# Kernel tuning notes

Measured on AMD Instinct MI355X. Metric: run time of the kernel, lower is better.

The kernel has to match this reference:

```python
import jax, jax.numpy as jnp
import numpy as np

N = 100000      # nodes
E = 1600000     # edges
D_IN = 256
D_HID = 256
D_OUT = 256
DROP_P = 0.5


def setup_inputs() -> dict:
    key = jax.random.key(0)
    ks = jax.random.split(key, 10)
    s = 1.0 / np.sqrt(D_HID)
    return {
        "z": jax.random.normal(ks[0], (N, D_OUT), jnp.float32),
        "omega": jax.random.normal(ks[1], (N, D_IN), jnp.float32),
        "edge_index": jax.random.randint(ks[2], (2, E), 0, N, jnp.int32),
        "W_lin": jax.random.normal(ks[3], (D_IN, D_HID), jnp.float32) * s,
        "b_lin": jnp.zeros((D_HID,), jnp.float32),
        "W_g1": jax.random.normal(ks[4], (D_HID, D_HID), jnp.float32) * s,
        "b_g1": jnp.zeros((D_HID,), jnp.float32),
        "W_g2": jax.random.normal(ks[5], (D_HID, D_OUT), jnp.float32) * s,
        "b_g2": jnp.zeros((D_OUT,), jnp.float32),
        "mask1": jax.random.bernoulli(ks[6], 1.0 - DROP_P, (N, D_HID)),
        "mask2": jax.random.bernoulli(ks[7], 1.0 - DROP_P, (N, D_HID)),
    }


def _gcn_norm(edge_index):
    # add self-loops, symmetric normalization deg^-1/2 * deg^-1/2
    loop = jnp.arange(N, dtype=edge_index.dtype)
    src = jnp.concatenate([edge_index[0], loop])
    dst = jnp.concatenate([edge_index[1], loop])
    deg = jax.ops.segment_sum(jnp.ones_like(dst, jnp.float32), dst, num_segments=N)
    dinv = jax.lax.rsqrt(deg)  # deg >= 1 because of self-loops
    norm = dinv[src] * dinv[dst]  # [E+N]
    return src, dst, norm


def _gcn_conv(x, W, b, src, dst, norm):
    h = x @ W                                  # [N, d_out]
    msg = h[src] * norm[:, None]               # gather over edges
    out = jax.ops.segment_sum(msg, dst, num_segments=N)  # scatter-add
    return out + b


def _dropout(x, mask):
    return jnp.where(mask, x * (1.0 / (1.0 - DROP_P)), 0.0)


def reference(z, omega, edge_index, W_lin, b_lin, W_g1, b_g1, W_g2, b_g2, mask1, mask2):
    src, dst, norm = _gcn_norm(edge_index)
    # layer 0: Linear + relu + dropout
    h = _dropout(jax.nn.relu(omega @ W_lin + b_lin), mask1)
    # layer 1: GCNConv + relu + dropout
    h = _dropout(jax.nn.relu(_gcn_conv(h, W_g1, b_g1, src, dst, norm)), mask2)
    # layer 2: GCNConv
    h = _gcn_conv(h, W_g2, b_g2, src, dst, norm)
    return z * h
```

## Files before the change

kernel.cpp:

```cpp
#include <hip/hip_runtime.h>
#include <stdint.h>

#define NN 100000
#define EE 1600000
#define DD 256

typedef __bf16 bf16;
typedef __attribute__((ext_vector_type(8))) __bf16 bf16x8;
typedef __attribute__((ext_vector_type(4))) float f32x4;
typedef __attribute__((ext_vector_type(4))) unsigned int u32x4;
typedef __attribute__((ext_vector_type(8))) unsigned short u16x8;

typedef __attribute__((address_space(1))) const unsigned int g_u32c;
typedef __attribute__((address_space(3))) unsigned int lds_u32;

__device__ __forceinline__ float bflo(unsigned int u) {
    union { unsigned int u; float f; } x; x.u = u << 16; return x.f;
}
__device__ __forceinline__ float bfhi(unsigned int u) {
    union { unsigned int u; float f; } x; x.u = u & 0xFFFF0000u; return x.f;
}
__device__ __forceinline__ unsigned short f2bf(float f) {
    return __builtin_bit_cast(unsigned short, (__bf16)f);
}

#define NSUB 128
__global__ __launch_bounds__(256) void count_deg_k(
    const int* __restrict__ dst, int* __restrict__ cnt) {
    int bid = blockIdx.x;
    int prt = bid & 7;
    int sub = bid >> 3;
    int lo = prt * (NN >> 3);
    int hi = (prt == 7) ? NN : lo + (NN >> 3);
    const int per = EE / NSUB;
    int e0 = sub * per;
    int e1 = (sub == NSUB - 1) ? EE : e0 + per;
    for (int e = e0 + threadIdx.x; e < e1; e += 256) {
        int d = dst[e];
        if (d >= lo && d < hi) atomicAdd(&cnt[d], 1);
    }
}
__global__ __launch_bounds__(256) void scan_blk_k(const int* __restrict__ cnt,
                                                  int* __restrict__ part,
                                                  int* __restrict__ bsum,
                                                  float* __restrict__ dinv) {
    __shared__ int buf[256];
    int i = blockIdx.x * 256 + threadIdx.x;
    int v = 0;
    if (i < NN) { v = cnt[i] + 1; dinv[i] = rsqrtf((float)v); }
    buf[threadIdx.x] = v;
    __syncthreads();
    for (int off = 1; off < 256; off <<= 1) {
        int t = (threadIdx.x >= off) ? buf[threadIdx.x - off] : 0;
        __syncthreads();
        buf[threadIdx.x] += t;
        __syncthreads();
    }
    if (i < NN) part[i] = buf[threadIdx.x];
    if (threadIdx.x == 255) bsum[blockIdx.x] = buf[255];
}
__global__ __launch_bounds__(512) void scan_top_k(const int* __restrict__ bsum,
                                                  int* __restrict__ bpre, int nb) {
    __shared__ int buf[512];
    int v = (threadIdx.x < (unsigned)nb) ? bsum[threadIdx.x] : 0;
    buf[threadIdx.x] = v;
    __syncthreads();
    for (int off = 1; off < 512; off <<= 1) {
        int t = (threadIdx.x >= off) ? buf[threadIdx.x - off] : 0;
        __syncthreads();
        buf[threadIdx.x] += t;
        __syncthreads();
    }
    if (threadIdx.x < (unsigned)nb) bpre[threadIdx.x] = buf[threadIdx.x] - v;
}
__global__ void scan_fin_k(const int* __restrict__ part, const int* __restrict__ bpre,
                           const int* __restrict__ cnt,
                           int* __restrict__ offs, int* __restrict__ cur,
                           int* __restrict__ cs) {
    int i = blockIdx.x * 256 + threadIdx.x;
    if (i >= NN) return;
    int o1 = part[i] + bpre[blockIdx.x];
    offs[i + 1] = o1;
    if (i == 0) offs[0] = 0;
    int o = o1 - (cnt[i] + 1);
    cs[o] = i;
    cur[i] = o + 1;
}
__global__ __launch_bounds__(256) void fill_csr_k(
    const int* __restrict__ src, const int* __restrict__ dst,
    int* __restrict__ cur, int* __restrict__ cs) {
    int bid = blockIdx.x;
    int prt = bid & 7;
    int sub = bid >> 3;
    int lo = prt * (NN >> 3);
    int hi = (prt == 7) ? NN : lo + (NN >> 3);
    const int per = EE / NSUB;
    int e0 = sub * per;
    int e1 = (sub == NSUB - 1) ? EE : e0 + per;
    for (int e = e0 + threadIdx.x; e < e1; e += 256) {
        int d = dst[e];
        if (d >= lo && d < hi) {
            int s = src[e];
            int pos = atomicAdd(&cur[d], 1);
            cs[pos] = s;
        }
    }
}

__global__ __launch_bounds__(256) void prep_k(
    const float* __restrict__ W0, const float* __restrict__ W1, const float* __restrict__ W2,
    bf16* __restrict__ T0, bf16* __restrict__ T1, bf16* __restrict__ T2,
    const unsigned int* __restrict__ m, int* __restrict__ flag) {
    int b = blockIdx.x;
    if (b == 192) {
        if (threadIdx.x < 64) {
            unsigned int v = m[threadIdx.x];
            int bad = (v > 1u && v != 0x3F800000u) ? 1 : 0;
            unsigned long long bl = __ballot(bad);
            if (threadIdx.x == 0) *flag = (bl != 0ull) ? 1 : 0;
        }
        return;
    }
    const float* W = b < 64 ? W0 : (b < 128 ? W1 : W2);
    bf16*       T  = b < 64 ? T0 : (b < 128 ? T1 : T2);
    int bb = b & 63;
    __shared__ float tile[32][33];
    int bx = bb & 7, by = bb >> 3;
    int tx = threadIdx.x & 31, ty = threadIdx.x >> 5;
    #pragma unroll
    for (int r = 0; r < 32; r += 8)
        tile[ty + r][tx] = W[(size_t)(by * 32 + ty + r) * DD + bx * 32 + tx];
    __syncthreads();
    #pragma unroll
    for (int r = 0; r < 32; r += 8)
        T[(size_t)(bx * 32 + ty + r) * DD + by * 32 + tx] = (bf16)tile[tx][ty + r];
}

template <int ID, int EPI, int F32A>
__global__ __launch_bounds__(256) void gemm_k(
    const void* __restrict__ Ap, const bf16* __restrict__ Wt,
    const float* __restrict__ bias, const void* __restrict__ mask,
    const int* __restrict__ flagp, const float* __restrict__ z,
    const float* __restrict__ dinv, void* __restrict__ outp) {
    __shared__ __align__(16) bf16 As[64 * 64];
    __shared__ __align__(16) bf16 Bs[256 * 64];

    int m0 = blockIdx.x * 64;
    if (m0 >= NN) return;
    int tid = threadIdx.x;
    int wid = tid >> 6, lane = tid & 63;
    int lr = lane & 15, lk = lane >> 4;
    int rx = lr & 7;

    f32x4 acc[4][4] = {};

    for (int k0 = 0; k0 < DD; k0 += 64) {
        #pragma unroll
        for (int i = 0; i < 2; i++) {
            int f = i * 256 + tid;
            int row = f >> 3;
            int cl  = f & 7;
            int cg  = cl ^ (row & 7);
            int gr = m0 + row; if (gr > NN - 1) gr = NN - 1;
            if (F32A) {
                const float* sp = (const float*)Ap + (size_t)gr * DD + k0 + cl * 8;
                float4 v0 = *(const float4*)sp;
                float4 v1 = *(const float4*)(sp + 4);
                u16x8 o = { f2bf(v0.x), f2bf(v0.y), f2bf(v0.z), f2bf(v0.w),
                            f2bf(v1.x), f2bf(v1.y), f2bf(v1.z), f2bf(v1.w) };
                *(u16x8*)(As + row * 64 + cg * 8) = o;
            } else {
                __builtin_amdgcn_global_load_lds(
                    (g_u32c*)((const bf16*)Ap + (size_t)gr * DD + k0 + cg * 8),
                    (lds_u32*)(As + (size_t)f * 8), 16, 0, 0);
            }
        }
        #pragma unroll
        for (int i = 0; i < 8; i++) {
            int f = i * 256 + tid;
            int row = f >> 3;
            int cg  = (f & 7) ^ (row & 7);
            __builtin_amdgcn_global_load_lds(
                (g_u32c*)(Wt + (size_t)row * DD + k0 + cg * 8),
                (lds_u32*)(Bs + (size_t)f * 8), 16, 0, 0);
        }
        __syncthreads();
        #pragma unroll
        for (int kk = 0; kk < 2; kk++) {
            bf16x8 af[4], bfr[4];
            #pragma unroll
            for (int mi = 0; mi < 4; mi++)
                af[mi] = *(const bf16x8*)(As + (mi * 16 + lr) * 64 + (((kk * 4 + lk) ^ rx) * 8));
            #pragma unroll
            for (int ni = 0; ni < 4; ni++)
                bfr[ni] = *(const bf16x8*)(Bs + (wid * 64 + ni * 16 + lr) * 64 + (((kk * 4 + lk) ^ rx) * 8));
            #pragma unroll
            for (int mi = 0; mi < 4; mi++)
                #pragma unroll
                for (int ni = 0; ni < 4; ni++)
                    acc[mi][ni] = __builtin_amdgcn_mfma_f32_16x16x32_bf16(
                        bfr[ni], af[mi], acc[mi][ni], 0, 0, 0);
        }
        __syncthreads();
    }

    int bm = (EPI == 1) ? *flagp : 0;
    #pragma unroll
    for (int mi = 0; mi < 4; mi++) {
        int gr = m0 + mi * 16 + lr;
        if (gr >= NN) continue;
        float ds = (EPI == 1) ? dinv[gr] : 0.f;
        #pragma unroll
        for (int ni = 0; ni < 4; ni++) {
            int gc = wid * 64 + ni * 16 + lk * 4;
            size_t idx = (size_t)gr * DD + gc;
            float4 b4 = *(const float4*)(bias + gc);
            float v0 = acc[mi][ni][0] + b4.x;
            float v1 = acc[mi][ni][1] + b4.y;
            float v2 = acc[mi][ni][2] + b4.z;
            float v3 = acc[mi][ni][3] + b4.w;
            if (EPI == 1) {
                v0 = fmaxf(v0, 0.f); v1 = fmaxf(v1, 0.f);
                v2 = fmaxf(v2, 0.f); v3 = fmaxf(v3, 0.f);
                if (bm) {
                    uchar4 u = *(const uchar4*)((const unsigned char*)mask + idx);
                    v0 *= u.x ? 2.f : 0.f; v1 *= u.y ? 2.f : 0.f;
                    v2 *= u.z ? 2.f : 0.f; v3 *= u.w ? 2.f : 0.f;
                } else {
                    uint4 u = *(const uint4*)((const unsigned int*)mask + idx);
                    v0 *= u.x ? 2.f : 0.f; v1 *= u.y ? 2.f : 0.f;
                    v2 *= u.z ? 2.f : 0.f; v3 *= u.w ? 2.f : 0.f;
                }
                v0 *= ds; v1 *= ds; v2 *= ds; v3 *= ds;
                ushort4 o = { f2bf(v0), f2bf(v1), f2bf(v2), f2bf(v3) };
                *(ushort4*)((unsigned short*)outp + idx) = o;
            } else {
                f32x4 zz = __builtin_nontemporal_load((const f32x4*)(z + idx));
                f32x4 o = { v0 * zz.x, v1 * zz.y, v2 * zz.z, v3 * zz.w };
                __builtin_nontemporal_store(o, (f32x4*)((float*)outp + idx));
            }
        }
    }
}

#define AGG_GET(J, UVAR, MVAR)                                                   \
    {                                                                            \
        int _i = 2 * (J) + half;                                                 \
        int _s = __shfl(sl, _i & 63);                                            \
        MVAR = (_i < nume) ? 1.f : 0.f;                                          \
        UVAR = *(const u32x4*)(tb + (((size_t)(unsigned)_s) << 9) + lcoff);      \
    }
#define AGG_FMA(UVAR, MVAR)                                                      \
    {                                                                            \
        acc[0] = fmaf(MVAR, bflo(UVAR.x), acc[0]);                               \
        acc[1] = fmaf(MVAR, bfhi(UVAR.x), acc[1]);                               \
        acc[2] = fmaf(MVAR, bflo(UVAR.y), acc[2]);                               \
        acc[3] = fmaf(MVAR, bfhi(UVAR.y), acc[3]);                               \
        acc[4] = fmaf(MVAR, bflo(UVAR.z), acc[4]);                               \
        acc[5] = fmaf(MVAR, bfhi(UVAR.z), acc[5]);                               \
        acc[6] = fmaf(MVAR, bflo(UVAR.w), acc[6]);                               \
        acc[7] = fmaf(MVAR, bfhi(UVAR.w), acc[7]);                               \
    }

__global__ __launch_bounds__(256) void agg_k(
    const bf16* __restrict__ t, const int* __restrict__ offs,
    const int* __restrict__ cs, const float* __restrict__ dinv,
    bf16* __restrict__ out) {
    int node = blockIdx.x * 4 + (threadIdx.x >> 6);
    if (node >= NN) return;
    int lane = threadIdx.x & 63;
    int half = lane >> 5;
    int lc = lane & 31;
    int beg = offs[node], end = offs[node + 1];

    float acc[8] = {};
    const char* tb = (const char*)t;
    size_t lcoff = (size_t)(lc << 4);

    for (int base = beg; base < end; base += 64) {
        int nume = min(64, end - base);
        int sl = 0;
        if (lane < nume) sl = __builtin_nontemporal_load(cs + base + lane);
        int nit = (nume + 1) >> 1;

        u32x4 ua, ub, uc, ud;
        float ma, mb, mc, md;
        AGG_GET(0, ua, ma);
        AGG_GET(1, ub, mb);
        AGG_GET(2, uc, mc);
        int j = 0;
        for (; j + 3 < nit; j += 4) {
            AGG_GET(j + 3, ud, md); AGG_FMA(ua, ma);
            AGG_GET(j + 4, ua, ma); AGG_FMA(ub, mb);
            AGG_GET(j + 5, ub, mb); AGG_FMA(uc, mc);
            AGG_GET(j + 6, uc, mc); AGG_FMA(ud, md);
        }
        int rem = nit - j;
        if (rem > 0) AGG_FMA(ua, ma);
        if (rem > 1) AGG_FMA(ub, mb);
        if (rem > 2) AGG_FMA(uc, mc);
    }

    float dn = dinv[node];
    #pragma unroll
    for (int i = 0; i < 8; i++) {
        acc[i] += __shfl_xor(acc[i], 32);
        acc[i] *= dn;
    }
    if (half == 0) {
        u16x8 o = { f2bf(acc[0]), f2bf(acc[1]), f2bf(acc[2]), f2bf(acc[3]),
                    f2bf(acc[4]), f2bf(acc[5]), f2bf(acc[6]), f2bf(acc[7]) };
        __builtin_nontemporal_store(o, (u16x8*)((unsigned short*)out + (size_t)node * DD + lc * 8));
    }
}

extern "C" void kernel_launch(void* const* d_in, const int* in_sizes, int n_in,
                              void* d_out, int out_size, void* d_ws, size_t ws_size,
                              hipStream_t stream) {
    const float* z     = (const float*)d_in[0];
    const float* omega = (const float*)d_in[1];
    const int*   eidx  = (const int*)d_in[2];
    const float* W_lin = (const float*)d_in[3];
    const float* b_lin = (const float*)d_in[4];
    const float* W_g1  = (const float*)d_in[5];
    const float* b_g1  = (const float*)d_in[6];
    const float* W_g2  = (const float*)d_in[7];
    const float* b_g2  = (const float*)d_in[8];
    const void*  mask1 = d_in[9];
    const void*  mask2 = d_in[10];

    const int* e_src = eidx;
    const int* e_dst = eidx + EE;

    char* p = (char*)d_ws;
    size_t off = 0;
    auto alloc = [&](size_t bytes) -> char* {
        char* r = p + off;
        off = (off + bytes + 255) & ~(size_t)255;
        return r;
    };
    const int NB256 = (NN + 255) / 256;
    int*   flag = (int*)  alloc(4);
    int*   cnt  = (int*)  alloc((size_t)NN * 4);
    int*   offs = (int*)  alloc(((size_t)NN + 1) * 4);
    int*   cur  = (int*)  alloc((size_t)NN * 4);
    int*   part = (int*)  alloc((size_t)NN * 4);
    int*   bsum = (int*)  alloc(512 * 4);
    int*   bpre = (int*)  alloc(512 * 4);
    float* dinv = (float*)alloc((size_t)NN * 4);
    int*   cs   = (int*)  alloc((size_t)(EE + NN) * 4);
    bf16*  WtL  = (bf16*) alloc((size_t)DD * DD * 2);
    bf16*  Wt1  = (bf16*) alloc((size_t)DD * DD * 2);
    bf16*  Wt2  = (bf16*) alloc((size_t)DD * DD * 2);
    const size_t NBH = (size_t)NN * DD * 2;
    bf16*  S1   = (bf16*) alloc(NBH);
    bf16*  S2   = (bf16*) alloc(NBH);

    (void)hipMemsetAsync(cnt, 0, (size_t)NN * 4, stream);
    count_deg_k<<<NSUB * 8, 256, 0, stream>>>(e_dst, cnt);
    scan_blk_k <<<NB256, 256, 0, stream>>>(cnt, part, bsum, dinv);
    scan_top_k <<<1, 512, 0, stream>>>(bsum, bpre, NB256);
    scan_fin_k <<<NB256, 256, 0, stream>>>(part, bpre, cnt, offs, cur, cs);
    fill_csr_k <<<NSUB * 8, 256, 0, stream>>>(e_src, e_dst, cur, cs);

    prep_k<<<193, 256, 0, stream>>>(W_lin, W_g1, W_g2, WtL, Wt1, Wt2,
                                    (const unsigned int*)mask1, flag);

    const int GB = (NN + 63) / 64;
    gemm_k<0, 1, 1><<<GB, 256, 0, stream>>>(omega, WtL, b_lin, mask1, flag, nullptr, dinv, S1);
    agg_k<<<NN / 4, 256, 0, stream>>>(S1, offs, cs, dinv, S2);
    gemm_k<1, 1, 0><<<GB, 256, 0, stream>>>(S2, Wt1, b_g1, mask2, flag, nullptr, dinv, S1);
    agg_k<<<NN / 4, 256, 0, stream>>>(S1, offs, cs, dinv, S2);
    gemm_k<2, 2, 0><<<GB, 256, 0, stream>>>(S2, Wt2, b_g2, nullptr, flag, z, dinv, d_out);
}
```

Measured before the change: 602.7 us.

## Fuse degree counting with first GEMM and move source dinv scaling into aggregation

```diff
diff --git a/kernel.cpp b/kernel.cpp
--- a/kernel.cpp
+++ b/kernel.cpp
@@ -4,6 +4,8 @@
 #define NN 100000
 #define EE 1600000
 #define DD 256
+#define GB0 1563
+#define NCNT 1024
 
 typedef __bf16 bf16;
 typedef __attribute__((ext_vector_type(8))) __bf16 bf16x8;
@@ -25,21 +27,6 @@
 }
 
 #define NSUB 128
-__global__ __launch_bounds__(256) void count_deg_k(
-    const int* __restrict__ dst, int* __restrict__ cnt) {
-    int bid = blockIdx.x;
-    int prt = bid & 7;
-    int sub = bid >> 3;
-    int lo = prt * (NN >> 3);
-    int hi = (prt == 7) ? NN : lo + (NN >> 3);
-    const int per = EE / NSUB;
-    int e0 = sub * per;
-    int e1 = (sub == NSUB - 1) ? EE : e0 + per;
-    for (int e = e0 + threadIdx.x; e < e1; e += 256) {
-        int d = dst[e];
-        if (d >= lo && d < hi) atomicAdd(&cnt[d], 1);
-    }
-}
 __global__ __launch_bounds__(256) void scan_blk_k(const int* __restrict__ cnt,
                                                   int* __restrict__ part,
                                                   int* __restrict__ bsum,
@@ -136,17 +123,12 @@
         T[(size_t)(bx * 32 + ty + r) * DD + by * 32 + tx] = (bf16)tile[tx][ty + r];
 }
 
-template <int ID, int EPI, int F32A>
-__global__ __launch_bounds__(256) void gemm_k(
+template <int EPI, int F32A>
+__device__ __forceinline__ void gemm_body(
     const void* __restrict__ Ap, const bf16* __restrict__ Wt,
     const float* __restrict__ bias, const void* __restrict__ mask,
     const int* __restrict__ flagp, const float* __restrict__ z,
-    const float* __restrict__ dinv, void* __restrict__ outp) {
-    __shared__ __align__(16) bf16 As[64 * 64];
-    __shared__ __align__(16) bf16 Bs[256 * 64];
-
-    int m0 = blockIdx.x * 64;
-    if (m0 >= NN) return;
+    void* __restrict__ outp, bf16* As, bf16* Bs, int m0) {
     int tid = threadIdx.x;
     int wid = tid >> 6, lane = tid & 63;
     int lr = lane & 15, lk = lane >> 4;
@@ -209,7 +191,6 @@
     for (int mi = 0; mi < 4; mi++) {
         int gr = m0 + mi * 16 + lr;
         if (gr >= NN) continue;
-        float ds = (EPI == 1) ? dinv[gr] : 0.f;
         #pragma unroll
         for (int ni = 0; ni < 4; ni++) {
             int gc = wid * 64 + ni * 16 + lk * 4;
@@ -231,7 +212,6 @@
                     v0 *= u.x ? 2.f : 0.f; v1 *= u.y ? 2.f : 0.f;
                     v2 *= u.z ? 2.f : 0.f; v3 *= u.w ? 2.f : 0.f;
                 }
-                v0 *= ds; v1 *= ds; v2 *= ds; v3 *= ds;
                 ushort4 o = { f2bf(v0), f2bf(v1), f2bf(v2), f2bf(v3) };
                 *(ushort4*)((unsigned short*)outp + idx) = o;
             } else {
@@ -243,11 +223,51 @@
     }
 }
 
+__global__ __launch_bounds__(256) void g0cnt_k(
+    const float* __restrict__ omega, const bf16* __restrict__ Wt,
+    const float* __restrict__ bias, const void* __restrict__ mask,
+    const int* __restrict__ flagp, bf16* __restrict__ outp,
+    const int* __restrict__ dst, int* __restrict__ cnt) {
+    __shared__ __align__(16) bf16 As[64 * 64];
+    __shared__ __align__(16) bf16 Bs[256 * 64];
+    int b = blockIdx.x;
+    if (b < NCNT) {
+        int prt = b & 7;
+        int sub = b >> 3;
+        int lo = prt * (NN >> 3);
+        int hi = (prt == 7) ? NN : lo + (NN >> 3);
+        const int per = EE / NSUB;
+        int e0 = sub * per;
+        int e1 = (sub == NSUB - 1) ? EE : e0 + per;
+        for (int e = e0 + threadIdx.x; e < e1; e += 256) {
+            int d = dst[e];
+            if (d >= lo && d < hi) atomicAdd(&cnt[d], 1);
+        }
+        return;
+    }
+    gemm_body<1, 1>(omega, Wt, bias, mask, flagp, nullptr, outp, As, Bs,
+                    (b - NCNT) * 64);
+}
+
+template <int ID, int EPI>
+__global__ __launch_bounds__(256) void gemm_k(
+    const bf16* __restrict__ Ap, const bf16* __restrict__ Wt,
+    const float* __restrict__ bias, const void* __restrict__ mask,
+    const int* __restrict__ flagp, const float* __restrict__ z,
+    void* __restrict__ outp) {
+    __shared__ __align__(16) bf16 As[64 * 64];
+    __shared__ __align__(16) bf16 Bs[256 * 64];
+    int m0 = blockIdx.x * 64;
+    if (m0 >= NN) return;
+    gemm_body<EPI, 0>(Ap, Wt, bias, mask, flagp, z, outp, As, Bs, m0);
+}
+
 #define AGG_GET(J, UVAR, MVAR)                                                   \
     {                                                                            \
         int _i = 2 * (J) + half;                                                 \
         int _s = __shfl(sl, _i & 63);                                            \
-        MVAR = (_i < nume) ? 1.f : 0.f;                                          \
+        float _w = __shfl(wl, _i & 63);                                          \
+        MVAR = (_i < nume) ? _w : 0.f;                                           \
         UVAR = *(const u32x4*)(tb + (((size_t)(unsigned)_s) << 9) + lcoff);      \
     }
 #define AGG_FMA(UVAR, MVAR)                                                      \
@@ -279,8 +299,11 @@
 
     for (int base = beg; base < end; base += 64) {
         int nume = min(64, end - base);
-        int sl = 0;
-        if (lane < nume) sl = __builtin_nontemporal_load(cs + base + lane);
+        int sl = 0; float wl = 0.f;
+        if (lane < nume) {
+            sl = __builtin_nontemporal_load(cs + base + lane);
+            wl = dinv[sl];
+        }
         int nit = (nume + 1) >> 1;
 
         u32x4 ua, ub, uc, ud;
@@ -357,19 +380,20 @@
     bf16*  S2   = (bf16*) alloc(NBH);
 
     (void)hipMemsetAsync(cnt, 0, (size_t)NN * 4, stream);
-    count_deg_k<<<NSUB * 8, 256, 0, stream>>>(e_dst, cnt);
+    prep_k<<<193, 256, 0, stream>>>(W_lin, W_g1, W_g2, WtL, Wt1, Wt2,
+                                    (const unsigned int*)mask1, flag);
+
+    g0cnt_k<<<NCNT + GB0, 256, 0, stream>>>(omega, WtL, b_lin, mask1, flag,
+                                            S1, e_dst, cnt);
+
     scan_blk_k <<<NB256, 256, 0, stream>>>(cnt, part, bsum, dinv);
     scan_top_k <<<1, 512, 0, stream>>>(bsum, bpre, NB256);
     scan_fin_k <<<NB256, 256, 0, stream>>>(part, bpre, cnt, offs, cur, cs);
     fill_csr_k <<<NSUB * 8, 256, 0, stream>>>(e_src, e_dst, cur, cs);
 
-    prep_k<<<193, 256, 0, stream>>>(W_lin, W_g1, W_g2, WtL, Wt1, Wt2,
-                                    (const unsigned int*)mask1, flag);
-
-    const int GB = (NN + 63) / 64;
-    gemm_k<0, 1, 1><<<GB, 256, 0, stream>>>(omega, WtL, b_lin, mask1, flag, nullptr, dinv, S1);
+    const int GB = GB0;
     agg_k<<<NN / 4, 256, 0, stream>>>(S1, offs, cs, dinv, S2);
-    gemm_k<1, 1, 0><<<GB, 256, 0, stream>>>(S2, Wt1, b_g1, mask2, flag, nullptr, dinv, S1);
+    gemm_k<1, 1><<<GB, 256, 0, stream>>>(S2, Wt1, b_g1, mask2, flag, nullptr, S1);
     agg_k<<<NN / 4, 256, 0, stream>>>(S1, offs, cs, dinv, S2);
-    gemm_k<2, 2, 0><<<GB, 256, 0, stream>>>(S2, Wt2, b_g2, nullptr, flag, z, dinv, d_out);
-}
+    gemm_k<2, 2><<<GB, 256, 0, stream>>>(S2, Wt2, b_g2, nullptr, flag, z, d_out);
+}
```

Result: no change. 597.0 us (-0.9%).
